# Kernel tuning notes

Measured on AMD Instinct MI355X. Metric: run time of the kernel, lower is better.

## Reference

```python
import jax, jax.numpy as jnp
import numpy as np

N, F_IN, H1, NHEADS, H2, H3 = 4096, 512, 128, 4, 256, 64
ALPHA = 0.2
NEG = -9e15


def setup_inputs() -> dict:
    key = jax.random.key(0)
    k_x, k_adj, k_watt, k_a, k_w1, k_w2 = jax.random.split(key, 6)
    x = jax.random.normal(k_x, (N, F_IN), dtype=jnp.float32)
    adj = (jax.random.uniform(k_adj, (N, N)) < 0.004).astype(jnp.float32)
    adj = adj.at[jnp.arange(N), jnp.arange(N)].set(1.0)
    # xavier-ish init scales
    W_att = jax.random.normal(k_watt, (NHEADS, F_IN, H1), dtype=jnp.float32) * (1.0 / np.sqrt(F_IN))
    a = jax.random.normal(k_a, (NHEADS, 2 * H1), dtype=jnp.float32) * 0.1
    W1 = jax.random.normal(k_w1, (NHEADS * H1, H2), dtype=jnp.float32) * (1.0 / np.sqrt(NHEADS * H1))
    W2 = jax.random.normal(k_w2, (H2, H3), dtype=jnp.float32) * (1.0 / np.sqrt(H2))
    return {"x": x, "adj": adj, "W_att": W_att, "a": a, "W1": W1, "W2": W2}


def reference(x, adj, W_att, a, W1, W2):
    h1 = W_att.shape[-1]
    # --- multi-head GAT (dense masked attention, faithful to source) ---
    Wh = jnp.einsum('nf,hfo->hno', x, W_att)              # [H, N, h1]
    a1, a2 = a[:, :h1], a[:, h1:]                          # each [H, h1]
    s1 = jnp.einsum('hno,ho->hn', Wh, a1)                  # [H, N]
    s2 = jnp.einsum('hno,ho->hn', Wh, a2)                  # [H, N]
    e = jax.nn.leaky_relu(s1[:, :, None] + s2[:, None, :], ALPHA)  # [H, N, N]
    att = jax.nn.softmax(jnp.where(adj[None] > 0, e, NEG), axis=-1)
    h = jnp.einsum('hnm,hmo->hno', att, Wh)                # [H, N, h1]
    xcat = jnp.transpose(h, (1, 0, 2)).reshape(x.shape[0], -1)  # [N, H*h1]
    xr = jax.nn.relu(xcat)
    # --- GCN layers: support = x @ W; out = adj @ support ---
    g1 = jax.nn.relu(adj @ (xr @ W1))                      # [N, H2]
    g2 = adj @ (g1 @ W2)                                   # [N, H3]
    return g2, jax.nn.softmax(g2, axis=1)
```

## Files before the change

kernel.cpp:

```cpp
#include <hip/hip_runtime.h>
#include <hip/hip_bf16.h>

#define NN    4096
#define FIN   512
#define NH1   128
#define NH    4
#define NH2   256
#define NH3   64
#define CAP   64
#define ALPHA 0.2f

typedef float f32x4 __attribute__((ext_vector_type(4)));
typedef __bf16 bf16x8 __attribute__((ext_vector_type(8)));

__device__ __forceinline__ unsigned short f2bf(float f) {
    union { float f; unsigned u; } x; x.f = f;
    unsigned r = x.u + 0x7fff + ((x.u >> 16) & 1);
    return (unsigned short)(r >> 16);
}
__device__ __forceinline__ float bf2f(ushort u) {
    union { unsigned u; float f; } x; x.u = ((unsigned)u) << 16;
    return x.f;
}
__device__ __forceinline__ float bflo(unsigned w) {
    union { unsigned u; float f; } x; x.u = w << 16; return x.f;
}
__device__ __forceinline__ float bfhi(unsigned w) {
    union { unsigned u; float f; } x; x.u = w & 0xffff0000u; return x.f;
}

#define C_X     2048
#define C_WATT  (C_X + 1024)
#define C_W1T   (C_WATT + 512)
#define C_W2B   (C_W1T + 16)
#define C_Z     (C_W2B + 32)

__global__ __launch_bounds__(256) void k_conv(
    const float* __restrict__ x, ushort* __restrict__ xb,
    const float* __restrict__ W_att, ushort* __restrict__ Wattb,
    const float* __restrict__ W1, ushort* __restrict__ W1t,
    const float* __restrict__ W2, ushort* __restrict__ W2b,
    float* __restrict__ s1s2) {
    int bid = blockIdx.x;
    int tid = threadIdx.x;
    if (bid < C_X) {
        int i = (bid * 256 + tid) * 4;
        float4 v = *reinterpret_cast<const float4*>(x + i);
        ushort4 o;
        o.x = f2bf(v.x); o.y = f2bf(v.y); o.z = f2bf(v.z); o.w = f2bf(v.w);
        *reinterpret_cast<ushort4*>(xb + i) = o;
    } else if (bid < C_WATT) {
        int idx = (bid - C_X) * 256 + tid;
        int col = idx >> 9, f = idx & 511;
        int h = col >> 7, o = col & 127;
        Wattb[idx] = f2bf(W_att[h * (FIN * NH1) + f * NH1 + o]);
    } else if (bid < C_W1T) {
        int idx = (bid - C_WATT) * 256 + tid;
        int c = idx >> 9, r = idx & 511;
        W1t[idx] = f2bf(W1[(size_t)r * NH2 + c]);
    } else if (bid < C_W2B) {
        int i = ((bid - C_W1T) * 256 + tid) * 4;
        float4 v = *reinterpret_cast<const float4*>(W2 + i);
        ushort4 o;
        o.x = f2bf(v.x); o.y = f2bf(v.y); o.z = f2bf(v.z); o.w = f2bf(v.w);
        *reinterpret_cast<ushort4*>(W2b + i) = o;
    } else {
        int i = (bid - C_W2B) * 256 + tid;
        f32x4 z = {0.f, 0.f, 0.f, 0.f};
        *reinterpret_cast<f32x4*>(s1s2 + i * 4) = z;
    }
}

template <int SCORES, int MT, int BYBITS>
__global__ __launch_bounds__(256) void k_gemm(const ushort* __restrict__ A,
                                              const ushort* __restrict__ Bt,
                                              ushort* __restrict__ Cb,
                                              const float* __restrict__ av,
                                              float* __restrict__ s1,
                                              float* __restrict__ s2,
                                              int M, int N, int K) {
    __shared__ ushort As[2][32 * MT * 64];
    __shared__ ushort Bs[2][64 * 64];
    const int tid = threadIdx.x;
    const int wid = tid >> 6;
    const int lane = tid & 63;
    const int bid = blockIdx.x;
    const int row0 = (bid & ((1 << BYBITS) - 1)) * (32 * MT);
    const int col0 = (bid >> BYBITS) * 64;
    const int wr = wid >> 1, wc = wid & 1;

    f32x4 acc[MT][2] = {};
    const int nt = K / 64;

    auto stage = [&](int buf, int k0) {
        #pragma unroll
        for (int j = 0; j < MT; ++j) {
            int ci = j * 256 + tid;
            int r = ci >> 3;
            int sc = (ci & 7) ^ (r & 7);
            const ushort* ga = A + (size_t)(row0 + r) * K + k0 + sc * 8;
            ushort* la = &As[buf][(size_t)ci * 8];
            __builtin_amdgcn_global_load_lds(
                (const __attribute__((address_space(1))) unsigned int*)ga,
                (__attribute__((address_space(3))) unsigned int*)la, 16, 0, 0);
        }
        #pragma unroll
        for (int j = 0; j < 2; ++j) {
            int ci = j * 256 + tid;
            int r = ci >> 3;
            int sc = (ci & 7) ^ (r & 7);
            const ushort* gb = Bt + (size_t)(col0 + r) * K + k0 + sc * 8;
            ushort* lb = &Bs[buf][(size_t)ci * 8];
            __builtin_amdgcn_global_load_lds(
                (const __attribute__((address_space(1))) unsigned int*)gb,
                (__attribute__((address_space(3))) unsigned int*)lb, 16, 0, 0);
        }
    };

    stage(0, 0);
    __syncthreads();
    int cur = 0;
    for (int t = 0; t < nt; ++t) {
        if (t + 1 < nt) stage(cur ^ 1, (t + 1) * 64);
        #pragma unroll
        for (int kk = 0; kk < 2; ++kk) {
            bf16x8 af[MT], bfv[2];
            #pragma unroll
            for (int m = 0; m < MT; ++m) {
                int r = wr * (16 * MT) + m * 16 + (lane & 15);
                int kc = kk * 4 + (lane >> 4);
                int off = r * 64 + (((kc ^ (r & 7)) & 7) << 3);
                af[m] = *reinterpret_cast<const bf16x8*>(&As[cur][off]);
            }
            #pragma unroll
            for (int n = 0; n < 2; ++n) {
                int c = wc * 32 + n * 16 + (lane & 15);
                int kc = kk * 4 + (lane >> 4);
                int off = c * 64 + (((kc ^ (c & 7)) & 7) << 3);
                bfv[n] = *reinterpret_cast<const bf16x8*>(&Bs[cur][off]);
            }
            #pragma unroll
            for (int m = 0; m < MT; ++m)
                #pragma unroll
                for (int n = 0; n < 2; ++n)
                    acc[m][n] = __builtin_amdgcn_mfma_f32_16x16x32_bf16(af[m], bfv[n], acc[m][n], 0, 0, 0);
        }
        __syncthreads();
        cur ^= 1;
    }
    #pragma unroll
    for (int m = 0; m < MT; ++m)
        #pragma unroll
        for (int n = 0; n < 2; ++n) {
            int col = col0 + wc * 32 + n * 16 + (lane & 15);
            #pragma unroll
            for (int j2 = 0; j2 < 4; ++j2) {
                int row = row0 + wr * (16 * MT) + m * 16 + (lane >> 4) * 4 + j2;
                Cb[(size_t)row * N + col] = f2bf(acc[m][n][j2]);
            }
        }
    if (SCORES) {
        int h = col0 >> 7;
        float a1v[2], a2v[2];
        #pragma unroll
        for (int n = 0; n < 2; ++n) {
            int colh = (col0 & 127) + wc * 32 + n * 16 + (lane & 15);
            a1v[n] = av[h * 256 + colh];
            a2v[n] = av[h * 256 + 128 + colh];
        }
        #pragma unroll
        for (int m = 0; m < MT; ++m)
            #pragma unroll
            for (int j2 = 0; j2 < 4; ++j2) {
                float v1 = acc[m][0][j2] * a1v[0] + acc[m][1][j2] * a1v[1];
                float v2 = acc[m][0][j2] * a2v[0] + acc[m][1][j2] * a2v[1];
                #pragma unroll
                for (int off = 1; off < 16; off <<= 1) {
                    v1 += __shfl_xor(v1, off);
                    v2 += __shfl_xor(v2, off);
                }
                if ((lane & 15) == 0) {
                    int row = row0 + wr * (16 * MT) + m * 16 + (lane >> 4) * 4 + j2;
                    atomicAdd(&s1[h * NN + row], v1);
                    atomicAdd(&s2[h * NN + row], v2);
                }
            }
    }
}

__global__ __launch_bounds__(256) void k_attn_csr(const float* __restrict__ adj,
                                                  const ushort* __restrict__ Whb,
                                                  const float* __restrict__ s1,
                                                  const float* __restrict__ s2,
                                                  int* __restrict__ nbr,
                                                  int* __restrict__ cnt,
                                                  ushort* __restrict__ xrb) {
    __shared__ int lds_list[4][64];
    __shared__ int lds_cnt[4];
    __shared__ int mlist[CAP];
    __shared__ int stot;
    int n = blockIdx.x;
    int tid = threadIdx.x;
    int wid = tid >> 6;
    int lane = tid & 63;

    const uint4* arow = (const uint4*)(adj + (size_t)n * NN);
    uint4 v[4];
    #pragma unroll
    for (int it = 0; it < 4; ++it) v[it] = arow[wid * 256 + it * 64 + lane];
    const unsigned long long below = (1ull << lane) - 1ull;
    int base = 0;
    #pragma unroll
    for (int it = 0; it < 4; ++it) {
        unsigned long long b0 = __ballot(v[it].x != 0u);
        unsigned long long b1 = __ballot(v[it].y != 0u);
        unsigned long long b2 = __ballot(v[it].z != 0u);
        unsigned long long b3 = __ballot(v[it].w != 0u);
        int pre = __popcll(b0 & below) + __popcll(b1 & below) +
                  __popcll(b2 & below) + __popcll(b3 & below);
        int col0 = wid * 1024 + it * 256 + lane * 4;
        int pos = base + pre;
        if (v[it].x != 0u) { if (pos < 64) lds_list[wid][pos] = col0;     ++pos; }
        if (v[it].y != 0u) { if (pos < 64) lds_list[wid][pos] = col0 + 1; ++pos; }
        if (v[it].z != 0u) { if (pos < 64) lds_list[wid][pos] = col0 + 2; ++pos; }
        if (v[it].w != 0u) { if (pos < 64) lds_list[wid][pos] = col0 + 3; ++pos; }
        base += __popcll(b0) + __popcll(b1) + __popcll(b2) + __popcll(b3);
    }
    if (lane == 0) lds_cnt[wid] = base;
    __syncthreads();
    int c0 = lds_cnt[0], c1 = lds_cnt[1], c2 = lds_cnt[2], c3 = lds_cnt[3];
    {
        int off = (wid > 0 ? c0 : 0) + (wid > 1 ? c1 : 0) + (wid > 2 ? c2 : 0);
        int my = lds_cnt[wid]; if (my > 64) my = 64;
        if (lane < my) {
            int gpos = off + lane;
            if (gpos < CAP) {
                mlist[gpos] = lds_list[wid][lane];
                nbr[n * CAP + gpos] = lds_list[wid][lane];
            }
        }
        if (tid == 0) {
            int tot = c0 + c1 + c2 + c3;
            stot = tot < CAP ? tot : CAP;
            cnt[n] = stot;
        }
    }
    __syncthreads();
    int c = stot;

    int h = wid;
    int m = mlist[lane < c ? lane : 0];
    float e = -1e30f;
    float s1n = s1[h * NN + n];
    if (lane < c) {
        float t = s1n + s2[h * NN + m];
        e = (t >= 0.0f) ? t : ALPHA * t;
    }
    float mx = e;
    #pragma unroll
    for (int off = 32; off; off >>= 1) mx = fmaxf(mx, __shfl_xor(mx, off));
    float p = (lane < c) ? __expf(e - mx) : 0.0f;
    float s = p;
    #pragma unroll
    for (int off = 32; off; off >>= 1) s += __shfl_xor(s, off);
    p /= s;
    const ushort* wb = Whb + h * 128 + 2 * lane;
    float acc0 = 0.0f, acc1 = 0.0f;
    int cp8 = (c + 7) & ~7;
    for (int j = 0; j < cp8; j += 8) {
        float pj[8]; int mj[8]; unsigned wj[8];
        #pragma unroll
        for (int u = 0; u < 8; ++u) {
            pj[u] = __shfl(p, j + u);
            mj[u] = __shfl(m, j + u);
        }
        #pragma unroll
        for (int u = 0; u < 8; ++u)
            wj[u] = *reinterpret_cast<const unsigned*>(wb + (size_t)mj[u] * 512);
        #pragma unroll
        for (int u = 0; u < 8; ++u) {
            acc0 = fmaf(pj[u], bflo(wj[u]), acc0);
            acc1 = fmaf(pj[u], bfhi(wj[u]), acc1);
        }
    }
    unsigned ow = (unsigned)f2bf(fmaxf(acc0, 0.0f)) | ((unsigned)f2bf(fmaxf(acc1, 0.0f)) << 16);
    *reinterpret_cast<unsigned*>(xrb + (size_t)n * 512 + h * 128 + 2 * lane) = ow;
}

__global__ __launch_bounds__(256) void k_g1y2(const ushort* __restrict__ y1b,
                                              const int* __restrict__ nbr,
                                              const int* __restrict__ cnt,
                                              const ushort* __restrict__ W2b,
                                              float* __restrict__ y2) {
    __shared__ float g1s[2][NH2];
    __shared__ float part[2][2][NH3];
    int half = threadIdx.x >> 7;
    int t = threadIdx.x & 127;
    int n = blockIdx.x * 2 + half;
    int c = cnt[n];
    const int* nb = nbr + n * CAP;
    {
        float acc0 = 0.0f, acc1 = 0.0f;
        const ushort* yb = y1b + 2 * t;
        for (int j = 0; j < c; j += 8) {
            int idx[8]; float f[8]; unsigned w[8];
            #pragma unroll
            for (int u = 0; u < 8; ++u) {
                idx[u] = nb[(j + u < c) ? j + u : j];
                f[u] = (j + u < c) ? 1.f : 0.f;
            }
            #pragma unroll
            for (int u = 0; u < 8; ++u)
                w[u] = *reinterpret_cast<const unsigned*>(yb + (size_t)idx[u] * NH2);
            #pragma unroll
            for (int u = 0; u < 8; ++u) {
                acc0 = fmaf(f[u], bflo(w[u]), acc0);
                acc1 = fmaf(f[u], bfhi(w[u]), acc1);
            }
        }
        g1s[half][2 * t]     = fmaxf(acc0, 0.0f);
        g1s[half][2 * t + 1] = fmaxf(acc1, 0.0f);
    }
    __syncthreads();
    int q = t >> 6, col = t & 63;
    float acc = 0.0f;
    #pragma unroll 8
    for (int i = 0; i < 128; ++i) {
        int k = q * 128 + i;
        acc = fmaf(g1s[half][k], bf2f(W2b[k * NH3 + col]), acc);
    }
    part[half][q][col] = acc;
    __syncthreads();
    if (t < 64)
        y2[(size_t)n * NH3 + t] = part[half][0][t] + part[half][1][t];
}

__global__ __launch_bounds__(256) void k_final(const float* __restrict__ Y2,
                                               const int* __restrict__ nbr,
                                               const int* __restrict__ cnt,
                                               float* __restrict__ out) {
    int n = blockIdx.x * 4 + (threadIdx.x >> 6);
    int lane = threadIdx.x & 63;
    int c = cnt[n];
    const int* nb = nbr + n * CAP;
    float acc = 0.0f;
    for (int j = 0; j < c; j += 8) {
        int idx[8]; float f[8]; float v[8];
        #pragma unroll
        for (int u = 0; u < 8; ++u) {
            idx[u] = nb[(j + u < c) ? j + u : j];
            f[u] = (j + u < c) ? 1.f : 0.f;
        }
        #pragma unroll
        for (int u = 0; u < 8; ++u)
            v[u] = Y2[(size_t)idx[u] * NH3 + lane];
        #pragma unroll
        for (int u = 0; u < 8; ++u)
            acc = fmaf(f[u], v[u], acc);
    }
    out[(size_t)n * NH3 + lane] = acc;
    float mx = acc;
    #pragma unroll
    for (int off = 32; off; off >>= 1) mx = fmaxf(mx, __shfl_xor(mx, off));
    float p = __expf(acc - mx);
    float s = p;
    #pragma unroll
    for (int off = 32; off; off >>= 1) s += __shfl_xor(s, off);
    out[(size_t)NN * NH3 + (size_t)n * NH3 + lane] = p / s;
}

extern "C" void kernel_launch(void* const* d_in, const int* in_sizes, int n_in,
                              void* d_out, int out_size, void* d_ws, size_t ws_size,
                              hipStream_t stream) {
    const float* x     = (const float*)d_in[0];
    const float* adj   = (const float*)d_in[1];
    const float* W_att = (const float*)d_in[2];
    const float* a     = (const float*)d_in[3];
    const float* W1    = (const float*)d_in[4];
    const float* W2    = (const float*)d_in[5];
    float* out = (float*)d_out;

    char* p = (char*)d_ws;
    ushort* xb    = (ushort*)p; p += (size_t)NN * FIN * 2;
    ushort* Wattb = (ushort*)p; p += (size_t)FIN * NH * NH1 * 2;
    ushort* W1t   = (ushort*)p; p += (size_t)NH2 * (NH * NH1) * 2;
    ushort* W2b   = (ushort*)p; p += (size_t)NH2 * NH3 * 2;
    ushort* Whb   = (ushort*)p; p += (size_t)NN * NH * NH1 * 2;
    float*  s1    = (float*)p;  p += (size_t)NH * NN * 4;
    float*  s2    = (float*)p;  p += (size_t)NH * NN * 4;
    int*    nbr   = (int*)p;    p += (size_t)NN * CAP * 4;
    int*    cnt   = (int*)p;    p += (size_t)NN * 4;
    ushort* xrb   = (ushort*)p; p += (size_t)NN * NH * NH1 * 2;
    ushort* y1b   = (ushort*)p; p += (size_t)NN * NH2 * 2;
    float*  y2    = (float*)p;  p += (size_t)NN * NH3 * 4;

    k_conv<<<C_Z, 256, 0, stream>>>(x, xb, W_att, Wattb, W1, W1t, W2, W2b, s1);
    k_gemm<1, 4, 5><<<256, 256, 0, stream>>>(
        xb, Wattb, Whb, a, s1, s2, NN, NH * NH1, FIN);
    k_attn_csr<<<NN, 256, 0, stream>>>(adj, Whb, s1, s2, nbr, cnt, xrb);
    k_gemm<0, 1, 7><<<512, 256, 0, stream>>>(
        xrb, W1t, y1b, nullptr, nullptr, nullptr, NN, NH2, NH * NH1);
    k_g1y2<<<NN / 2, 256, 0, stream>>>(y1b, nbr, cnt, W2b, y2);
    k_final<<<NN / 4, 256, 0, stream>>>(y2, nbr, cnt, out);
}
```

Before: 68.47 us.

## Fuse x fp32-to-bf16 conversion into first GEMM and retile it

The separate pass that converts x to bf16 in the conversion kernel is removed. The first GEMM now loads fp32 x through registers, converts it, and writes bf16 into LDS with a register-prefetch double buffer. Its tile shrinks from 128x64 to 64x64, giving 512 blocks instead of 256. This drops a 4096x512 write and re-read of bf16 x in exchange for more global load bytes per tile and register-staged A loads instead of direct-to-LDS loads. The second GEMM is specialised into its own non-templated kernel with no functional change.

```diff
diff --git a/kernel.cpp b/kernel.cpp
--- a/kernel.cpp
+++ b/kernel.cpp
@@ -29,28 +29,20 @@
     union { unsigned u; float f; } x; x.u = w & 0xffff0000u; return x.f;
 }
 
-#define C_X     2048
-#define C_WATT  (C_X + 1024)
+#define C_WATT  1024
 #define C_W1T   (C_WATT + 512)
 #define C_W2B   (C_W1T + 16)
 #define C_Z     (C_W2B + 32)
 
 __global__ __launch_bounds__(256) void k_conv(
-    const float* __restrict__ x, ushort* __restrict__ xb,
     const float* __restrict__ W_att, ushort* __restrict__ Wattb,
     const float* __restrict__ W1, ushort* __restrict__ W1t,
     const float* __restrict__ W2, ushort* __restrict__ W2b,
     float* __restrict__ s1s2) {
     int bid = blockIdx.x;
     int tid = threadIdx.x;
-    if (bid < C_X) {
-        int i = (bid * 256 + tid) * 4;
-        float4 v = *reinterpret_cast<const float4*>(x + i);
-        ushort4 o;
-        o.x = f2bf(v.x); o.y = f2bf(v.y); o.z = f2bf(v.z); o.w = f2bf(v.w);
-        *reinterpret_cast<ushort4*>(xb + i) = o;
-    } else if (bid < C_WATT) {
-        int idx = (bid - C_X) * 256 + tid;
+    if (bid < C_WATT) {
+        int idx = bid * 256 + tid;
         int col = idx >> 9, f = idx & 511;
         int h = col >> 7, o = col & 127;
         Wattb[idx] = f2bf(W_att[h * (FIN * NH1) + f * NH1 + o]);
@@ -71,39 +63,55 @@
     }
 }
 
-template <int SCORES, int MT, int BYBITS>
-__global__ __launch_bounds__(256) void k_gemm(const ushort* __restrict__ A,
-                                              const ushort* __restrict__ Bt,
-                                              ushort* __restrict__ Cb,
-                                              const float* __restrict__ av,
-                                              float* __restrict__ s1,
-                                              float* __restrict__ s2,
-                                              int M, int N, int K) {
-    __shared__ ushort As[2][32 * MT * 64];
+__global__ __launch_bounds__(256) void k_gemm1f(const float* __restrict__ X,
+                                                const ushort* __restrict__ Bt,
+                                                ushort* __restrict__ Cb,
+                                                const float* __restrict__ av,
+                                                float* __restrict__ s1,
+                                                float* __restrict__ s2) {
+    const int N = NH * NH1, K = FIN;
+    __shared__ ushort As[2][64 * 64];
     __shared__ ushort Bs[2][64 * 64];
     const int tid = threadIdx.x;
     const int wid = tid >> 6;
     const int lane = tid & 63;
     const int bid = blockIdx.x;
-    const int row0 = (bid & ((1 << BYBITS) - 1)) * (32 * MT);
-    const int col0 = (bid >> BYBITS) * 64;
+    const int row0 = (bid & 63) * 64;
+    const int col0 = (bid >> 6) * 64;
     const int wr = wid >> 1, wc = wid & 1;
 
-    f32x4 acc[MT][2] = {};
+    f32x4 acc[2][2] = {};
     const int nt = K / 64;
 
-    auto stage = [&](int buf, int k0) {
-        #pragma unroll
-        for (int j = 0; j < MT; ++j) {
+    float4 fa[2][2];
+    int cia[2];
+
+    auto issueA = [&](int k0) {
+        #pragma unroll
+        for (int j = 0; j < 2; ++j) {
             int ci = j * 256 + tid;
             int r = ci >> 3;
             int sc = (ci & 7) ^ (r & 7);
-            const ushort* ga = A + (size_t)(row0 + r) * K + k0 + sc * 8;
-            ushort* la = &As[buf][(size_t)ci * 8];
-            __builtin_amdgcn_global_load_lds(
-                (const __attribute__((address_space(1))) unsigned int*)ga,
-                (__attribute__((address_space(3))) unsigned int*)la, 16, 0, 0);
-        }
+            const float* ga = X + (size_t)(row0 + r) * K + k0 + sc * 8;
+            fa[j][0] = *reinterpret_cast<const float4*>(ga);
+            fa[j][1] = *reinterpret_cast<const float4*>(ga + 4);
+            cia[j] = ci;
+        }
+    };
+    auto writeA = [&](int buf) {
+        #pragma unroll
+        for (int j = 0; j < 2; ++j) {
+            ushort4 o0, o1;
+            o0.x = f2bf(fa[j][0].x); o0.y = f2bf(fa[j][0].y);
+            o0.z = f2bf(fa[j][0].z); o0.w = f2bf(fa[j][0].w);
+            o1.x = f2bf(fa[j][1].x); o1.y = f2bf(fa[j][1].y);
+            o1.z = f2bf(fa[j][1].z); o1.w = f2bf(fa[j][1].w);
+            ushort* la = &As[buf][(size_t)cia[j] * 8];
+            *reinterpret_cast<ushort4*>(la) = o0;
+            *reinterpret_cast<ushort4*>(la + 4) = o1;
+        }
+    };
+    auto stageB = [&](int buf, int k0) {
         #pragma unroll
         for (int j = 0; j < 2; ++j) {
             int ci = j * 256 + tid;
@@ -117,17 +125,22 @@
         }
     };
 
-    stage(0, 0);
+    issueA(0);
+    stageB(0, 0);
+    writeA(0);
     __syncthreads();
     int cur = 0;
     for (int t = 0; t < nt; ++t) {
-        if (t + 1 < nt) stage(cur ^ 1, (t + 1) * 64);
+        if (t + 1 < nt) {
+            issueA((t + 1) * 64);
+            stageB(cur ^ 1, (t + 1) * 64);
+        }
         #pragma unroll
         for (int kk = 0; kk < 2; ++kk) {
-            bf16x8 af[MT], bfv[2];
-            #pragma unroll
-            for (int m = 0; m < MT; ++m) {
-                int r = wr * (16 * MT) + m * 16 + (lane & 15);
+            bf16x8 af[2], bfv[2];
+            #pragma unroll
+            for (int m = 0; m < 2; ++m) {
+                int r = wr * 32 + m * 16 + (lane & 15);
                 int kc = kk * 4 + (lane >> 4);
                 int off = r * 64 + (((kc ^ (r & 7)) & 7) << 3);
                 af[m] = *reinterpret_cast<const bf16x8*>(&As[cur][off]);
@@ -140,51 +153,130 @@
                 bfv[n] = *reinterpret_cast<const bf16x8*>(&Bs[cur][off]);
             }
             #pragma unroll
-            for (int m = 0; m < MT; ++m)
+            for (int m = 0; m < 2; ++m)
                 #pragma unroll
                 for (int n = 0; n < 2; ++n)
                     acc[m][n] = __builtin_amdgcn_mfma_f32_16x16x32_bf16(af[m], bfv[n], acc[m][n], 0, 0, 0);
         }
+        if (t + 1 < nt) writeA(cur ^ 1);
         __syncthreads();
         cur ^= 1;
     }
     #pragma unroll
-    for (int m = 0; m < MT; ++m)
+    for (int m = 0; m < 2; ++m)
         #pragma unroll
         for (int n = 0; n < 2; ++n) {
             int col = col0 + wc * 32 + n * 16 + (lane & 15);
             #pragma unroll
             for (int j2 = 0; j2 < 4; ++j2) {
-                int row = row0 + wr * (16 * MT) + m * 16 + (lane >> 4) * 4 + j2;
+                int row = row0 + wr * 32 + m * 16 + (lane >> 4) * 4 + j2;
                 Cb[(size_t)row * N + col] = f2bf(acc[m][n][j2]);
             }
         }
-    if (SCORES) {
-        int h = col0 >> 7;
-        float a1v[2], a2v[2];
-        #pragma unroll
-        for (int n = 0; n < 2; ++n) {
-            int colh = (col0 & 127) + wc * 32 + n * 16 + (lane & 15);
-            a1v[n] = av[h * 256 + colh];
-            a2v[n] = av[h * 256 + 128 + colh];
-        }
-        #pragma unroll
-        for (int m = 0; m < MT; ++m)
-            #pragma unroll
-            for (int j2 = 0; j2 < 4; ++j2) {
-                float v1 = acc[m][0][j2] * a1v[0] + acc[m][1][j2] * a1v[1];
-                float v2 = acc[m][0][j2] * a2v[0] + acc[m][1][j2] * a2v[1];
-                #pragma unroll
-                for (int off = 1; off < 16; off <<= 1) {
-                    v1 += __shfl_xor(v1, off);
-                    v2 += __shfl_xor(v2, off);
-                }
-                if ((lane & 15) == 0) {
-                    int row = row0 + wr * (16 * MT) + m * 16 + (lane >> 4) * 4 + j2;
-                    atomicAdd(&s1[h * NN + row], v1);
-                    atomicAdd(&s2[h * NN + row], v2);
-                }
-            }
+    int h = col0 >> 7;
+    float a1v[2], a2v[2];
+    #pragma unroll
+    for (int n = 0; n < 2; ++n) {
+        int colh = (col0 & 127) + wc * 32 + n * 16 + (lane & 15);
+        a1v[n] = av[h * 256 + colh];
+        a2v[n] = av[h * 256 + 128 + colh];
+    }
+    #pragma unroll
+    for (int m = 0; m < 2; ++m)
+        #pragma unroll
+        for (int j2 = 0; j2 < 4; ++j2) {
+            float v1 = acc[m][0][j2] * a1v[0] + acc[m][1][j2] * a1v[1];
+            float v2 = acc[m][0][j2] * a2v[0] + acc[m][1][j2] * a2v[1];
+            #pragma unroll
+            for (int off = 1; off < 16; off <<= 1) {
+                v1 += __shfl_xor(v1, off);
+                v2 += __shfl_xor(v2, off);
+            }
+            if ((lane & 15) == 0) {
+                int row = row0 + wr * 32 + m * 16 + (lane >> 4) * 4 + j2;
+                atomicAdd(&s1[h * NN + row], v1);
+                atomicAdd(&s2[h * NN + row], v2);
+            }
+        }
+}
+
+__global__ __launch_bounds__(256) void k_gemm2(const ushort* __restrict__ A,
+                                               const ushort* __restrict__ Bt,
+                                               ushort* __restrict__ Cb,
+                                               int M, int N, int K) {
+    __shared__ ushort As[2][32 * 64];
+    __shared__ ushort Bs[2][64 * 64];
+    const int tid = threadIdx.x;
+    const int wid = tid >> 6;
+    const int lane = tid & 63;
+    const int bid = blockIdx.x;
+    const int row0 = (bid & 127) * 32;
+    const int col0 = (bid >> 7) * 64;
+    const int wr = wid >> 1, wc = wid & 1;
+
+    f32x4 acc[2] = {};
+    const int nt = K / 64;
+
+    auto stage = [&](int buf, int k0) {
+        {
+            int ci = tid;
+            int r = ci >> 3;
+            int sc = (ci & 7) ^ (r & 7);
+            const ushort* ga = A + (size_t)(row0 + r) * K + k0 + sc * 8;
+            ushort* la = &As[buf][(size_t)ci * 8];
+            __builtin_amdgcn_global_load_lds(
+                (const __attribute__((address_space(1))) unsigned int*)ga,
+                (__attribute__((address_space(3))) unsigned int*)la, 16, 0, 0);
+        }
+        #pragma unroll
+        for (int j = 0; j < 2; ++j) {
+            int ci = j * 256 + tid;
+            int r = ci >> 3;
+            int sc = (ci & 7) ^ (r & 7);
+            const ushort* gb = Bt + (size_t)(col0 + r) * K + k0 + sc * 8;
+            ushort* lb = &Bs[buf][(size_t)ci * 8];
+            __builtin_amdgcn_global_load_lds(
+                (const __attribute__((address_space(1))) unsigned int*)gb,
+                (__attribute__((address_space(3))) unsigned int*)lb, 16, 0, 0);
+        }
+    };
+
+    stage(0, 0);
+    __syncthreads();
+    int cur = 0;
+    for (int t = 0; t < nt; ++t) {
+        if (t + 1 < nt) stage(cur ^ 1, (t + 1) * 64);
+        #pragma unroll
+        for (int kk = 0; kk < 2; ++kk) {
+            bf16x8 af, bfv[2];
+            {
+                int r = wr * 16 + (lane & 15);
+                int kc = kk * 4 + (lane >> 4);
+                int off = r * 64 + (((kc ^ (r & 7)) & 7) << 3);
+                af = *reinterpret_cast<const bf16x8*>(&As[cur][off]);
+            }
+            #pragma unroll
+            for (int n = 0; n < 2; ++n) {
+                int c = wc * 32 + n * 16 + (lane & 15);
+                int kc = kk * 4 + (lane >> 4);
+                int off = c * 64 + (((kc ^ (c & 7)) & 7) << 3);
+                bfv[n] = *reinterpret_cast<const bf16x8*>(&Bs[cur][off]);
+            }
+            #pragma unroll
+            for (int n = 0; n < 2; ++n)
+                acc[n] = __builtin_amdgcn_mfma_f32_16x16x32_bf16(af, bfv[n], acc[n], 0, 0, 0);
+        }
+        __syncthreads();
+        cur ^= 1;
+    }
+    #pragma unroll
+    for (int n = 0; n < 2; ++n) {
+        int col = col0 + wc * 32 + n * 16 + (lane & 15);
+        #pragma unroll
+        for (int j2 = 0; j2 < 4; ++j2) {
+            int row = row0 + wr * 16 + (lane >> 4) * 4 + j2;
+            Cb[(size_t)row * N + col] = f2bf(acc[n][j2]);
+        }
     }
 }
 
@@ -381,7 +473,6 @@
     float* out = (float*)d_out;
 
     char* p = (char*)d_ws;
-    ushort* xb    = (ushort*)p; p += (size_t)NN * FIN * 2;
     ushort* Wattb = (ushort*)p; p += (size_t)FIN * NH * NH1 * 2;
     ushort* W1t   = (ushort*)p; p += (size_t)NH2 * (NH * NH1) * 2;
     ushort* W2b   = (ushort*)p; p += (size_t)NH2 * NH3 * 2;
@@ -394,12 +485,10 @@
     ushort* y1b   = (ushort*)p; p += (size_t)NN * NH2 * 2;
     float*  y2    = (float*)p;  p += (size_t)NN * NH3 * 4;
 
-    k_conv<<<C_Z, 256, 0, stream>>>(x, xb, W_att, Wattb, W1, W1t, W2, W2b, s1);
-    k_gemm<1, 4, 5><<<256, 256, 0, stream>>>(
-        xb, Wattb, Whb, a, s1, s2, NN, NH * NH1, FIN);
+    k_conv<<<C_Z, 256, 0, stream>>>(W_att, Wattb, W1, W1t, W2, W2b, s1);
+    k_gemm1f<<<512, 256, 0, stream>>>(x, Wattb, Whb, a, s1, s2);
     k_attn_csr<<<NN, 256, 0, stream>>>(adj, Whb, s1, s2, nbr, cnt, xrb);
-    k_gemm<0, 1, 7><<<512, 256, 0, stream>>>(
-        xrb, W1t, y1b, nullptr, nullptr, nullptr, NN, NH2, NH * NH1);
+    k_gemm2<<<512, 256, 0, stream>>>(xrb, W1t, y1b, NN, NH2, NH * NH1);
     k_g1y2<<<NN / 2, 256, 0, stream>>>(y1b, nbr, cnt, W2b, y2);
     k_final<<<NN / 4, 256, 0, stream>>>(y2, nbr, cnt, out);
 }
```

Result: faster. 66.80 us (-2.4%).
